# Optimization experiments

Hardware: AMD Instinct MI355X
Metric: run time of the kernel (lower is better)

Reference implementation:

```python
import jax, jax.numpy as jnp
import numpy as np

P_THRESH = 20  # p=0.2 * 100
# direction -> (di, dj): masked pixel (i,j) writes input[i,j] to x[i+di, j+dj], then avg to x[i,j]
OFFSETS = {0: (-1, -1), 1: (-1, 0), 2: (-1, 1), 3: (0, -1), 4: (0, 0), 5: (0, 1), 6: (1, -1), 7: (1, 0)}


def _shift(a, di, dj):
    """out[i+di, j+dj] = a[i, j] on last two axes; out-of-range -> 0/False."""
    H, W = a.shape[-2], a.shape[-1]
    pad = [(0, 0)] * (a.ndim - 2) + [(max(di, 0), max(-di, 0)), (max(dj, 0), max(-dj, 0))]
    p = jnp.pad(a, pad)
    sh, sw = max(-di, 0), max(-dj, 0)
    return p[..., sh:sh + H, sw:sw + W]


def _avg3x3_reflect(x):
    H, W = x.shape[-2], x.shape[-1]
    p = jnp.pad(x, [(0, 0), (0, 0), (1, 1), (1, 1)], mode='reflect')
    s = jnp.zeros_like(x)
    for i in range(3):
        for j in range(3):
            s = s + p[..., i:i + H, j:j + W]
    return s / 9.0


def brown_forward(input, dir, prob):
    avg = _avg3x3_reflect(input)
    pos = prob <= P_THRESH
    x = input
    for d in range(8):  # sequential, matching torch in-place write order
        di, dj = OFFSETS[d]
        m = (dir == d) & pos
        if d == 4:
            x = jnp.where(m, avg, x)  # mm: only avg write
        else:
            sm = _shift(m, di, dj)                       # neighbor-target mask
            x = jnp.where(sm, _shift(input, di, dj), x)  # x[i+di,j+dj] = input[i,j]
            mv = _shift(sm, -di, -dj)                    # mask restricted to valid region
            x = jnp.where(mv, avg, x)                    # x[i,j] = avg[i,j]
    return x


def setup_inputs() -> dict:
    key = jax.random.key(0)
    k1, k2, k3 = jax.random.split(key, 3)
    shape = (32, 64, 128, 128)
    return {
        'input': jax.random.normal(k1, shape, dtype=jnp.float32),
        'dir': jax.random.randint(k2, shape, 0, 8, dtype=jnp.int32),
        'prob': jax.random.randint(k3, shape, 1, 100, dtype=jnp.int32),
    }


def reference(input, dir, prob):
    return brown_forward(input, dir, prob)
```

## Files before the change

### kernel.cpp

```cpp
#include <hip/hip_runtime.h>
#include <cstddef>

#define H 128
#define W 128
#define TILE_R 32
#define LROWS (TILE_R + 2)
#define P_THRESH 20

typedef __attribute__((address_space(1))) const unsigned int glo_u32;
typedef __attribute__((address_space(3))) unsigned int lds_u32;

__global__ __launch_bounds__(256, 6)
void brown_kernel(const float* __restrict__ inp,
                  const int*  __restrict__ dirp,
                  const int*  __restrict__ prb,
                  float* __restrict__ out)
{
    __shared__ float        s_in[LROWS * W];
    __shared__ unsigned int s_mk[LROWS * 32];

    const int tid   = threadIdx.x;
    const int bid   = blockIdx.x;
    const int slice = bid >> 2;
    const int r0    = (bid & 3) * TILE_R;
    const size_t base = (size_t)slice * (size_t)(H * W);

    #pragma unroll
    for (int i = 0; i < 5; ++i) {
        const int idx = i * 256 + tid;
        if (idx < LROWS * 32) {
            const int L  = idx >> 5;
            const int c4 = idx & 31;
            const int gr = r0 - 1 + L;
            const int gri = (gr < 0) ? 1 : ((gr >= H) ? (H - 2) : gr);
            const float* gp = inp + base + (size_t)gri * W + c4 * 4;
            __builtin_amdgcn_global_load_lds((glo_u32*)gp, (lds_u32*)(s_in + idx * 4), 16, 0, 0);
            unsigned m;
            if (gr >= 0 && gr < H) {
                const int4 dv = ((const int4*)(dirp + base + (size_t)gr * W))[c4];
                const int4 pv = ((const int4*)(prb  + base + (size_t)gr * W))[c4];
                const unsigned a = (pv.x <= P_THRESH) ? (unsigned)dv.x : 8u;
                const unsigned b = (pv.y <= P_THRESH) ? (unsigned)dv.y : 8u;
                const unsigned c = (pv.z <= P_THRESH) ? (unsigned)dv.z : 8u;
                const unsigned d = (pv.w <= P_THRESH) ? (unsigned)dv.w : 8u;
                m = a | (b << 8) | (c << 16) | (d << 24);
            } else {
                m = 0x08080808u;
            }
            s_mk[idx] = m;
        }
    }
    __syncthreads();

    const int cq  = tid & 31;
    const int rg  = tid >> 5;
    const int j0  = cq << 2;
    const int lrb = rg << 2;
    const int cqm1 = (cq > 0)  ? cq - 1 : 0;
    const int cqp1 = (cq < 31) ? cq + 1 : 31;

    auto load_row = [&](int Lr, float v[6], unsigned& ma, unsigned& mb) {
        const float4 c      = ((const float4*)(s_in + Lr * W))[cq];
        const unsigned mwc  = s_mk[Lr * 32 + cq];
        const unsigned mwl  = s_mk[Lr * 32 + cqm1];
        const unsigned mwr  = s_mk[Lr * 32 + cqp1];
        const float lf = __shfl_up(c.w, 1);
        const float rt = __shfl_down(c.x, 1);
        v[1] = c.x; v[2] = c.y; v[3] = c.z; v[4] = c.w;
        v[0] = (cq > 0)  ? lf : c.y;
        v[5] = (cq < 31) ? rt : c.z;
        const unsigned ml = (cq > 0)  ? (mwl >> 24)   : 8u;
        const unsigned mr = (cq < 31) ? (mwr & 255u)  : 8u;
        ma = (mwc << 8) | ml;
        mb = (mwc >> 8) | (mr << 24);
    };

    float va[6], vb[6], vc[6];
    unsigned maa, mab, mba, mbb, mca, mcb;
    load_row(lrb + 0, va, maa, mab);
    load_row(lrb + 1, vb, mba, mbb);

    #pragma unroll
    for (int rr = 0; rr < 4; ++rr) {
        load_row(lrb + rr + 2, vc, mca, mcb);

        const int gi = r0 + lrb + rr;
        float cs[6];
        #pragma unroll
        for (int w = 0; w < 6; ++w) cs[w] = va[w] + vb[w] + vc[w];

        float4 res;
        float* rp = (float*)&res;
        #pragma unroll
        for (int p = 0; p < 4; ++p) {
            const float avg = (cs[p] + cs[p + 1] + cs[p + 2]) * (1.0f / 9.0f);
            const unsigned wTop = (p < 2) ? (maa >> (8 * p)) : (mab >> (8 * (p - 2)));
            const unsigned wMid = (p < 2) ? (mba >> (8 * p)) : (mbb >> (8 * (p - 2)));
            const unsigned wBot = (p < 2) ? (mca >> (8 * p)) : (mcb >> (8 * (p - 2)));

            float val = vb[p + 1];
            int dl = -1;
            if (((wBot >> 16) & 255u) == 0u) { val = vc[p + 2]; dl = 0; }
            if (((wBot >>  8) & 255u) == 1u) { val = vc[p + 1]; dl = 1; }
            if (( wBot        & 255u) == 2u) { val = vc[p];     dl = 2; }
            if (((wMid >> 16) & 255u) == 3u) { val = vb[p + 2]; dl = 3; }
            if (( wMid        & 255u) == 5u) { val = vb[p];     dl = 5; }
            if (((wTop >> 16) & 255u) == 6u) { val = va[p + 2]; dl = 6; }
            if (((wTop >>  8) & 255u) == 7u) { val = va[p + 1]; dl = 7; }

            const int msel = (int)((wMid >> 8) & 255u);
            const int q3 = (msel * 11) >> 5;
            const int di = q3 - 1;
            const int dj = msel - q3 * 3 - 1;
            const int ti = gi + di;
            const int tj = j0 + p + dj;
            const bool bok = (msel < 8) & ((unsigned)ti < 128u) & ((unsigned)tj < 128u);
            if (bok & (msel >= dl)) val = avg;
            rp[p] = val;
        }
        ((float4*)(out + base + (size_t)gi * W))[cq] = res;

        #pragma unroll
        for (int w = 0; w < 6; ++w) { va[w] = vb[w]; vb[w] = vc[w]; }
        maa = mba; mab = mbb; mba = mca; mbb = mcb;
    }
}

extern "C" void kernel_launch(void* const* d_in, const int* in_sizes, int n_in,
                              void* d_out, int out_size, void* d_ws, size_t ws_size,
                              hipStream_t stream) {
    const float* inp  = (const float*)d_in[0];
    const int*   dirp = (const int*)d_in[1];
    const int*   prb  = (const int*)d_in[2];
    float* out = (float*)d_out;

    const int slices = in_sizes[0] / (H * W);
    const int grid = slices * (H / TILE_R);
    brown_kernel<<<grid, 256, 0, stream>>>(inp, dirp, prb, out);
}
```

Before: 388.6 us.

## Drop LDS staging and load rows directly from global with shuffles

Removes the shared-memory tile and its block-wide barrier. Each thread now reads its six rows of input, dir and prob straight from global memory and gets neighbour masks through wave shuffles instead of LDS reads. This gets rid of the LDS traffic and the __syncthreads stall, and may raise occupancy. In exchange, the two halo rows each 4-row group needs are loaded redundantly from global (6 rows per 4 output rows), so dir/prob/input traffic grows and relies on the cache to absorb it.

```diff
diff --git a/kernel.cpp b/kernel.cpp
--- a/kernel.cpp
+++ b/kernel.cpp
@@ -4,11 +4,7 @@
 #define H 128
 #define W 128
 #define TILE_R 32
-#define LROWS (TILE_R + 2)
 #define P_THRESH 20
-
-typedef __attribute__((address_space(1))) const unsigned int glo_u32;
-typedef __attribute__((address_space(3))) unsigned int lds_u32;
 
 __global__ __launch_bounds__(256, 6)
 void brown_kernel(const float* __restrict__ inp,
@@ -16,75 +12,56 @@
                   const int*  __restrict__ prb,
                   float* __restrict__ out)
 {
-    __shared__ float        s_in[LROWS * W];
-    __shared__ unsigned int s_mk[LROWS * 32];
-
     const int tid   = threadIdx.x;
     const int bid   = blockIdx.x;
     const int slice = bid >> 2;
     const int r0    = (bid & 3) * TILE_R;
     const size_t base = (size_t)slice * (size_t)(H * W);
 
-    #pragma unroll
-    for (int i = 0; i < 5; ++i) {
-        const int idx = i * 256 + tid;
-        if (idx < LROWS * 32) {
-            const int L  = idx >> 5;
-            const int c4 = idx & 31;
-            const int gr = r0 - 1 + L;
-            const int gri = (gr < 0) ? 1 : ((gr >= H) ? (H - 2) : gr);
-            const float* gp = inp + base + (size_t)gri * W + c4 * 4;
-            __builtin_amdgcn_global_load_lds((glo_u32*)gp, (lds_u32*)(s_in + idx * 4), 16, 0, 0);
-            unsigned m;
-            if (gr >= 0 && gr < H) {
-                const int4 dv = ((const int4*)(dirp + base + (size_t)gr * W))[c4];
-                const int4 pv = ((const int4*)(prb  + base + (size_t)gr * W))[c4];
-                const unsigned a = (pv.x <= P_THRESH) ? (unsigned)dv.x : 8u;
-                const unsigned b = (pv.y <= P_THRESH) ? (unsigned)dv.y : 8u;
-                const unsigned c = (pv.z <= P_THRESH) ? (unsigned)dv.z : 8u;
-                const unsigned d = (pv.w <= P_THRESH) ? (unsigned)dv.w : 8u;
-                m = a | (b << 8) | (c << 16) | (d << 24);
-            } else {
-                m = 0x08080808u;
-            }
-            s_mk[idx] = m;
-        }
-    }
-    __syncthreads();
-
     const int cq  = tid & 31;
     const int rg  = tid >> 5;
     const int j0  = cq << 2;
-    const int lrb = rg << 2;
-    const int cqm1 = (cq > 0)  ? cq - 1 : 0;
-    const int cqp1 = (cq < 31) ? cq + 1 : 31;
+    const int gi0 = r0 + (rg << 2);
 
-    auto load_row = [&](int Lr, float v[6], unsigned& ma, unsigned& mb) {
-        const float4 c      = ((const float4*)(s_in + Lr * W))[cq];
-        const unsigned mwc  = s_mk[Lr * 32 + cq];
-        const unsigned mwl  = s_mk[Lr * 32 + cqm1];
-        const unsigned mwr  = s_mk[Lr * 32 + cqp1];
-        const float lf = __shfl_up(c.w, 1);
-        const float rt = __shfl_down(c.x, 1);
+    auto load_row = [&](int k, float v[6], unsigned& ma, unsigned& mb) {
+        const int gr  = gi0 - 1 + k;
+        const int gri = (gr < 0) ? 1 : ((gr >= H) ? (H - 2) : gr);
+        const float4 c = ((const float4*)(inp + base + (size_t)gri * W))[cq];
+        unsigned mwc;
+        if ((unsigned)gr < (unsigned)H) {
+            const int4 dv = ((const int4*)(dirp + base + (size_t)gr * W))[cq];
+            const int4 pv = ((const int4*)(prb  + base + (size_t)gr * W))[cq];
+            const unsigned a  = (pv.x <= P_THRESH) ? (unsigned)dv.x : 8u;
+            const unsigned b  = (pv.y <= P_THRESH) ? (unsigned)dv.y : 8u;
+            const unsigned cc = (pv.z <= P_THRESH) ? (unsigned)dv.z : 8u;
+            const unsigned d  = (pv.w <= P_THRESH) ? (unsigned)dv.w : 8u;
+            mwc = a | (b << 8) | (cc << 16) | (d << 24);
+        } else {
+            mwc = 0x08080808u;
+        }
+        const float    lf  = __shfl_up(c.w, 1);
+        const float    rt  = __shfl_down(c.x, 1);
+        const unsigned mwl = __shfl_up(mwc, 1);
+        const unsigned mwr = __shfl_down(mwc, 1);
         v[1] = c.x; v[2] = c.y; v[3] = c.z; v[4] = c.w;
         v[0] = (cq > 0)  ? lf : c.y;
         v[5] = (cq < 31) ? rt : c.z;
-        const unsigned ml = (cq > 0)  ? (mwl >> 24)   : 8u;
-        const unsigned mr = (cq < 31) ? (mwr & 255u)  : 8u;
+        const unsigned ml = (cq > 0)  ? (mwl >> 24)  : 8u;
+        const unsigned mr = (cq < 31) ? (mwr & 255u) : 8u;
         ma = (mwc << 8) | ml;
         mb = (mwc >> 8) | (mr << 24);
     };
 
     float va[6], vb[6], vc[6];
     unsigned maa, mab, mba, mbb, mca, mcb;
-    load_row(lrb + 0, va, maa, mab);
-    load_row(lrb + 1, vb, mba, mbb);
+    load_row(0, va, maa, mab);
+    load_row(1, vb, mba, mbb);
 
     #pragma unroll
     for (int rr = 0; rr < 4; ++rr) {
-        load_row(lrb + rr + 2, vc, mca, mcb);
+        load_row(rr + 2, vc, mca, mcb);
 
-        const int gi = r0 + lrb + rr;
+        const int gi = gi0 + rr;
         float cs[6];
         #pragma unroll
         for (int w = 0; w < 6; ++w) cs[w] = va[w] + vb[w] + vc[w];
```

Measured after the change: 405.6 us. 4.4% more time.
